# Kernel optimization log

Hardware: AMD Instinct MI355X
Metric: run time of the kernel (lower is better)

Reference implementation:

```python
import jax, jax.numpy as jnp
import numpy as np

D_IN, D_H, BATCH = 4096, 512, 8192


def _layernorm(x, g, b, eps=1e-5):
    mu = jnp.mean(x, axis=-1, keepdims=True)
    var = jnp.var(x, axis=-1, keepdims=True)
    return (x - mu) * jax.lax.rsqrt(var + eps) * g + b


def setup_inputs() -> dict:
    key = jax.random.key(0)
    ks = jax.random.split(key, 10)
    x = jax.random.normal(ks[0], (BATCH, D_IN), jnp.float32)
    h = jax.random.normal(ks[1], (BATCH, D_H), jnp.float32)
    s1 = 1.0 / np.sqrt(D_IN + D_H)
    W1 = jax.random.uniform(ks[2], (D_IN + D_H, D_H), jnp.float32, -s1, s1)
    b1 = jnp.zeros((D_H,), jnp.float32)
    ln1_g = jnp.ones((D_H,), jnp.float32)
    ln1_b = jnp.zeros((D_H,), jnp.float32)
    s2 = 1.0 / np.sqrt(D_H)
    W2 = jax.random.uniform(ks[3], (D_H, 3 * D_H), jnp.float32, -s2, s2)
    b2 = jnp.zeros((3 * D_H,), jnp.float32)
    base_tau = jnp.ones((D_H,), jnp.float32)  # time_constant_init = 1.0
    base_A = jax.random.normal(ks[4], (D_H, D_H), jnp.float32) * 0.1
    idx = jnp.arange(D_H)
    base_A = base_A.at[idx, idx].set(-0.5)
    base_B = jax.random.normal(ks[5], (D_IN, D_H), jnp.float32) * 0.1
    hn_g = jnp.ones((D_H,), jnp.float32)
    hn_b = jnp.zeros((D_H,), jnp.float32)
    return {"x": x, "h": h, "W1": W1, "b1": b1, "ln1_g": ln1_g, "ln1_b": ln1_b,
            "W2": W2, "b2": b2, "base_tau": base_tau, "base_A": base_A,
            "base_B": base_B, "hn_g": hn_g, "hn_b": hn_b}


def reference(x, h, W1, b1, ln1_g, ln1_b, W2, b2, base_tau, base_A, base_B, hn_g, hn_b):
    dt = 0.1
    # time_net hypernetwork
    xh = jnp.concatenate([x, h], axis=-1)                 # [B, D_IN+D_H]
    t = _layernorm(xh @ W1 + b1, ln1_g, ln1_b)
    t = jax.nn.gelu(t, approximate=False)
    params = t @ W2 + b2                                  # [B, 3*D_H]
    tau_s, A_s, B_s = jnp.split(params, 3, axis=-1)
    tau = base_tau * (jax.nn.sigmoid(tau_s) * 2.0)        # [B, D_H]
    A_row = 1.0 + 0.5 * jnp.tanh(A_s)                     # per-sample row scale of A
    B_col = 1.0 + 0.5 * jnp.tanh(B_s)                     # per-sample col scale of B
    # A[b] = base_A * A_row[b][:,None]; h @ A[b].T == (h @ base_A.T) * A_row[b]
    recurrent = (h @ base_A.T) * A_row                    # [B, D_H]
    # B[b] = base_B * B_col[b][None,:]; x @ B[b] == (x @ base_B) * B_col[b]
    input_term = (x @ base_B) * B_col                     # [B, D_H]
    dhdt = -h / (tau + 1e-8) + jnp.tanh(recurrent + input_term)
    new_h = _layernorm(h + dt * dhdt, hn_g, hn_b)
    return new_h
```

## Files before the change

kernel.cpp:

```cpp
#include <hip/hip_runtime.h>

#define BATCH 8192
#define DIN 4096
#define DH 512

typedef float f32x4 __attribute__((ext_vector_type(4)));
typedef float f32x2 __attribute__((ext_vector_type(2)));
typedef short s16x8 __attribute__((ext_vector_type(8)));
typedef unsigned short u16x2 __attribute__((ext_vector_type(2)));
typedef unsigned short u16x4 __attribute__((ext_vector_type(4)));
typedef unsigned short u16x8 __attribute__((ext_vector_type(8)));

static __device__ __forceinline__ unsigned short f2bf(float f) {
  unsigned int u = __float_as_uint(f);
  u += 0x7FFFu + ((u >> 16) & 1u);
  return (unsigned short)(u >> 16);
}
static __device__ __forceinline__ float bf2f(unsigned short s) {
  return __uint_as_float(((unsigned int)s) << 16);
}

typedef const __attribute__((address_space(1))) unsigned int* gas_ptr;
typedef __attribute__((address_space(3))) unsigned int* las_ptr;
static __device__ __forceinline__ void gl_lds16(const unsigned short* g, unsigned short* l) {
  __builtin_amdgcn_global_load_lds((gas_ptr)g, (las_ptr)l, 16, 0, 0);
}

static __device__ __forceinline__ void transpose_body(
    const float* __restrict__ in, int C,
    unsigned short* __restrict__ out, int ldo, int row_off,
    int bx, int by, float (*tl)[33])
{
  const int tid = threadIdx.x;
  const int tx = tid & 31, ty = tid >> 5;
  const int c0 = bx * 32, r0 = by * 32;
#pragma unroll
  for (int i = 0; i < 4; i++)
    tl[ty + 8 * i][tx] = in[(size_t)(r0 + ty + 8 * i) * C + c0 + tx];
  __syncthreads();
#pragma unroll
  for (int i = 0; i < 4; i++)
    out[(size_t)(row_off + c0 + ty + 8 * i) * ldo + r0 + tx] = f2bf(tl[tx][ty + 8 * i]);
}

__global__ __launch_bounds__(256) void prep_all_k(
    const float* __restrict__ x, unsigned short* __restrict__ xbf,
    const float* __restrict__ h, unsigned short* __restrict__ hbf,
    const float* __restrict__ base_A, unsigned short* __restrict__ Abf,
    const float* __restrict__ W1, const float* __restrict__ base_B,
    unsigned short* __restrict__ BTcat,
    const float* __restrict__ W2, unsigned short* __restrict__ W2T)
{
  __shared__ float tl[32][33];
  const int b = blockIdx.x;
  const int tid = threadIdx.x;
  const int KC = DIN + DH;
  if (b < 32768) {
    const int i = (b * 256 + tid) * 4;
    f32x4 v = *(const f32x4*)(x + i);
    u16x4 p = { f2bf(v[0]), f2bf(v[1]), f2bf(v[2]), f2bf(v[3]) };
    *(u16x4*)(xbf + i) = p;
  } else if (b < 36864) {
    const int i = ((b - 32768) * 256 + tid) * 4;
    f32x4 v = *(const f32x4*)(h + i);
    u16x4 p = { f2bf(v[0]), f2bf(v[1]), f2bf(v[2]), f2bf(v[3]) };
    *(u16x4*)(hbf + i) = p;
  } else if (b < 37120) {
    const int i = ((b - 36864) * 256 + tid) * 4;
    f32x4 v = *(const f32x4*)(base_A + i);
    u16x4 p = { f2bf(v[0]), f2bf(v[1]), f2bf(v[2]), f2bf(v[3]) };
    *(u16x4*)(Abf + i) = p;
  } else if (b < 39424) {
    const int bb = b - 37120;
    transpose_body(W1, DH, BTcat, KC, 0, bb & 15, bb >> 4, tl);
  } else if (b < 41472) {
    const int bb = b - 39424;
    transpose_body(base_B, DH, BTcat, KC, DH, bb & 15, bb >> 4, tl);
  } else if (b < 41600) {
    const int gid = (b - 41472) * 256 + tid;
    const int row = gid >> 6, c = (gid & 63) * 8;
    u16x8 z = { 0, 0, 0, 0, 0, 0, 0, 0 };
    *(u16x8*)(BTcat + (size_t)(DH + row) * KC + DIN + c) = z;
  } else {
    const int bb = b - 41600;
    transpose_body(W2, 3 * DH, W2T, DH, 0, bb % 48, bb / 48, tl);
  }
}

template<int EPI>
static __device__ __forceinline__ void gemm3_engine(
    const unsigned short* __restrict__ A0, int lda0, int K0,
    const unsigned short* __restrict__ A1, int lda1,
    const unsigned short* __restrict__ BT, int ldb,
    unsigned short* __restrict__ C0, int ldc,
    unsigned short* __restrict__ C1,
    const float* __restrict__ bias,
    const float* __restrict__ base_tau,
    int mb, int nb, int K, char* smem)
{
  unsigned short* As = (unsigned short*)smem;
  unsigned short* Bs = (unsigned short*)(smem + 16384);

  const int tid = threadIdx.x;
  const int lane = tid & 63;
  const int wid = tid >> 6;
  const int wm = (wid >> 2) * 64;
  const int wn = (wid & 3) * 64;
  const int srow = lane >> 2;
  const int scol = ((lane & 3) ^ ((lane >> 3) & 3)) * 8;
  const int fr = lane & 15;
  const int fk = ((lane >> 4) ^ ((lane >> 1) & 3)) * 8;
  const int NT = K / 32;
  const int cw = wid * 3;

  f32x4 acc[4][4];
#pragma unroll
  for (int i = 0; i < 4; i++)
#pragma unroll
    for (int j = 0; j < 4; j++)
      acc[i][j] = (f32x4){ 0.f, 0.f, 0.f, 0.f };

  auto STAGE1 = [&](int buf, int t, int j) {
    const int c = cw + j;
    const int k0 = t * 32;
    if (c < 8) {
      const bool s0 = (k0 < K0);
      const unsigned short* Ab = s0 ? A0 : A1;
      const int ld = s0 ? lda0 : lda1;
      const int ko = (s0 ? k0 : k0 - K0) + scol;
      gl_lds16(Ab + (size_t)(mb + c * 16 + srow) * ld + ko,
               As + buf * 4096 + c * 512);
    } else {
      gl_lds16(BT + (size_t)(nb + (c - 8) * 16 + srow) * ldb + k0 + scol,
               Bs + buf * 8192 + (c - 8) * 512);
    }
  };

  STAGE1(0, 0, 0); STAGE1(0, 0, 1); STAGE1(0, 0, 2);
  asm volatile("s_waitcnt vmcnt(0)" ::: "memory");
  __builtin_amdgcn_s_barrier();

  int buf = 0;
  for (int t = 0; t < NT; t++) {
    const unsigned short* ar = As + buf * 4096;
    const unsigned short* br = Bs + buf * 8192;
    s16x8 af[4], bv0, bv1, bv2, bv3;
#pragma unroll
    for (int mi = 0; mi < 4; mi++)
      af[mi] = *(const s16x8*)(ar + (wm + mi * 16 + fr) * 32 + fk);
    bv0 = *(const s16x8*)(br + (wn + 0 * 16 + fr) * 32 + fk);
    bv1 = *(const s16x8*)(br + (wn + 1 * 16 + fr) * 32 + fk);

    if (t + 1 < NT) { STAGE1(buf ^ 1, t + 1, 0); STAGE1(buf ^ 1, t + 1, 1); }

    __builtin_amdgcn_s_setprio(1);
#pragma unroll
    for (int mi = 0; mi < 4; mi++)
      acc[mi][0] = __builtin_amdgcn_mfma_f32_16x16x32_bf16(af[mi], bv0, acc[mi][0], 0, 0, 0);
#pragma unroll
    for (int mi = 0; mi < 4; mi++)
      acc[mi][1] = __builtin_amdgcn_mfma_f32_16x16x32_bf16(af[mi], bv1, acc[mi][1], 0, 0, 0);
    __builtin_amdgcn_s_setprio(0);
    __builtin_amdgcn_s_barrier();

    bv2 = *(const s16x8*)(br + (wn + 2 * 16 + fr) * 32 + fk);
    bv3 = *(const s16x8*)(br + (wn + 3 * 16 + fr) * 32 + fk);
    if (t + 1 < NT) STAGE1(buf ^ 1, t + 1, 2);

    __builtin_amdgcn_s_setprio(1);
#pragma unroll
    for (int mi = 0; mi < 4; mi++)
      acc[mi][2] = __builtin_amdgcn_mfma_f32_16x16x32_bf16(af[mi], bv2, acc[mi][2], 0, 0, 0);
#pragma unroll
    for (int mi = 0; mi < 4; mi++)
      acc[mi][3] = __builtin_amdgcn_mfma_f32_16x16x32_bf16(af[mi], bv3, acc[mi][3], 0, 0, 0);
    __builtin_amdgcn_s_setprio(0);

    asm volatile("s_waitcnt vmcnt(0) lgkmcnt(0)" ::: "memory");
    __builtin_amdgcn_sched_barrier(0);
    __builtin_amdgcn_s_barrier();
    buf ^= 1;
  }

  const int rb = (lane >> 4) * 4;
#pragma unroll
  for (int mi = 0; mi < 4; mi++) {
#pragma unroll
    for (int ni = 0; ni < 4; ni++) {
#pragma unroll
      for (int r = 0; r < 4; r++) {
        const int row = mb + wm + mi * 16 + rb + r;
        const int col = nb + wn + ni * 16 + fr;
        float v = acc[mi][ni][r];
        if (EPI == 3) {
          if (col < DH) C0[(size_t)row * DH + col] = f2bf(v + bias[col]);
          else          C1[(size_t)row * DH + (col - DH)] = f2bf(v);
        } else if (EPI == 2) {
          C0[(size_t)row * ldc + col] = f2bf(v);
        } else if (EPI == 1) {
          v += bias[col];
          if ((col >> 9) == 0) {
            const float s = 1.0f / (1.0f + expf(-v));
            v = 1.0f / (base_tau[col & (DH - 1)] * 2.0f * s + 1e-8f);
          } else {
            v = 1.0f + 0.5f * tanhf(v);
          }
          C0[(size_t)row * ldc + col] = f2bf(v);
        }
      }
    }
  }
}

template<int EPI>
static __device__ __forceinline__ void gemm2_engine(
    const unsigned short* __restrict__ A0, int lda0, int K0,
    const unsigned short* __restrict__ A1, int lda1,
    const unsigned short* __restrict__ BT, int ldb,
    unsigned short* __restrict__ C0, int ldc,
    unsigned short* __restrict__ C1,
    const float* __restrict__ bias,
    const float* __restrict__ base_tau,
    int mb, int nb, int K, char* smem)
{
  unsigned short* As = (unsigned short*)smem;
  unsigned short* Bs = (unsigned short*)(smem + 32768);
  float* red = (float*)smem;

  const int tid = threadIdx.x;
  const int lane = tid & 63;
  const int wid = tid >> 6;
  const int grp = wid >> 2;
  const int wg  = wid & 3;
  const int wm = (wg >> 1) * 64;
  const int wn = (wg & 1) * 64;
  const int srow = lane >> 2;
  const int scol = ((lane & 3) ^ ((lane >> 3) & 3)) * 8;
  const int fr = lane & 15;
  const int fk = ((lane >> 4) ^ ((lane >> 1) & 3)) * 8;
  const int NT2 = K / 64;

  f32x4 acc[4][4];
#pragma unroll
  for (int i = 0; i < 4; i++)
#pragma unroll
    for (int j = 0; j < 4; j++)
      acc[i][j] = (f32x4){ 0.f, 0.f, 0.f, 0.f };

  auto STAGE_A = [&](int buf, int per) {
    const int k0 = (2 * per + grp) * 32;
    const bool s0 = (k0 < K0);
    const unsigned short* Ab = s0 ? A0 : A1;
    const int ld = s0 ? lda0 : lda1;
    const int ko = (s0 ? k0 : k0 - K0) + scol;
    unsigned short* ab = As + (grp * 2 + buf) * 4096 + (32 * wg) * 32;
#pragma unroll
    for (int c = 0; c < 2; c++) {
      const int r = 32 * wg + c * 16 + srow;
      gl_lds16(Ab + (size_t)(mb + r) * ld + ko, ab + c * 16 * 32);
    }
  };
  auto STAGE_B = [&](int buf, int per) {
    const int k0 = (2 * per + grp) * 32;
    unsigned short* bb = Bs + (grp * 2 + buf) * 4096 + (32 * wg) * 32;
#pragma unroll
    for (int c = 0; c < 2; c++) {
      const int r = 32 * wg + c * 16 + srow;
      gl_lds16(BT + (size_t)(nb + r) * ldb + k0 + scol, bb + c * 16 * 32);
    }
  };

  STAGE_A(0, 0);
  STAGE_B(0, 0);
  asm volatile("s_waitcnt vmcnt(0)" ::: "memory");
  __builtin_amdgcn_s_barrier();

  int buf = 0;
  for (int t = 0; t < NT2; t++) {
    const unsigned short* ar = As + (grp * 2 + buf) * 4096;
    const unsigned short* br = Bs + (grp * 2 + buf) * 4096;
    s16x8 af[4], bv[4];
#pragma unroll
    for (int mi = 0; mi < 4; mi++)
      af[mi] = *(const s16x8*)(ar + (wm + mi * 16 + fr) * 32 + fk);
    bv[0] = *(const s16x8*)(br + (wn + fr) * 32 + fk);

#pragma unroll
    for (int p = 0; p < 4; p++) {
      if (p < 3)
        bv[p + 1] = *(const s16x8*)(br + (wn + (p + 1) * 16 + fr) * 32 + fk);
      if (p == 0 && t + 1 < NT2) STAGE_A(buf ^ 1, t + 1);
      if (p == 1 && t + 1 < NT2) STAGE_B(buf ^ 1, t + 1);

      __builtin_amdgcn_s_setprio(1);
#pragma unroll
      for (int mi = 0; mi < 4; mi++)
        acc[mi][p] = __builtin_amdgcn_mfma_f32_16x16x32_bf16(
            af[mi], bv[p], acc[mi][p], 0, 0, 0);
      __builtin_amdgcn_s_setprio(0);

      if (p == 3) {
        asm volatile("s_waitcnt vmcnt(0) lgkmcnt(0)" ::: "memory");
        __builtin_amdgcn_sched_barrier(0);
      }
      __builtin_amdgcn_s_barrier();
    }
    buf ^= 1;
  }

  if (grp == 1) {
#pragma unroll
    for (int mi = 0; mi < 4; mi++)
#pragma unroll
      for (int ni = 0; ni < 4; ni++)
        *(f32x4*)(red + (((wg * 4 + mi) * 4 + ni) * 64 + lane) * 4) = acc[mi][ni];
  }
  __syncthreads();
  if (grp != 0) return;

  const int rb = (lane >> 4) * 4;
#pragma unroll
  for (int mi = 0; mi < 4; mi++) {
#pragma unroll
    for (int ni = 0; ni < 4; ni++) {
      f32x4 o = *(const f32x4*)(red + (((wg * 4 + mi) * 4 + ni) * 64 + lane) * 4);
      acc[mi][ni] += o;
#pragma unroll
      for (int r = 0; r < 4; r++) {
        const int row = mb + wm + mi * 16 + rb + r;
        const int col = nb + wn + ni * 16 + fr;
        float v = acc[mi][ni][r];
        if (EPI == 2) {
          C0[(size_t)row * ldc + col] = f2bf(v);
        } else if (EPI == 1) {
          v += bias[col];
          if ((col >> 9) == 0) {
            const float s = 1.0f / (1.0f + expf(-v));
            v = 1.0f / (base_tau[col & (DH - 1)] * 2.0f * s + 1e-8f);
          } else {
            v = 1.0f + 0.5f * tanhf(v);
          }
          C0[(size_t)row * ldc + col] = f2bf(v);
        }
      }
    }
  }
}

__global__ __launch_bounds__(512) void fused_gemm_k(
    const unsigned short* __restrict__ xbf,
    const unsigned short* __restrict__ hbf,
    const unsigned short* __restrict__ BTcat,
    unsigned short* __restrict__ pre1,
    unsigned short* __restrict__ rawB,
    const float* __restrict__ b1)
{
  __shared__ __align__(16) char smem[49152];
  const int cpx = gridDim.x >> 3;
  const int virt = (blockIdx.x & 7) * cpx + (blockIdx.x >> 3);
  const int mb = (virt & 63) * 128;
  const int nb = (virt >> 6) * 256;
  gemm3_engine<3>(xbf, DIN, DIN, hbf, DH, BTcat, DIN + DH,
                  pre1, DH, rawB, b1, nullptr, mb, nb, DIN + DH, smem);
}

__global__ __launch_bounds__(512, 4) void tail_gemm_k(
    const unsigned short* __restrict__ hbf,
    const unsigned short* __restrict__ Abf,
    const unsigned short* __restrict__ tbf,
    const unsigned short* __restrict__ W2T,
    unsigned short* __restrict__ rawA,
    unsigned short* __restrict__ scales,
    const float* __restrict__ b2,
    const float* __restrict__ base_tau)
{
  __shared__ __align__(16) char smem[65536];
  const int b = blockIdx.x;
  if (b < 768) {
    const int mb = (b & 63) * 128, nb = (b >> 6) * 128;
    gemm2_engine<1>(tbf, DH, DH, nullptr, 0, W2T, DH,
                    scales, 3 * DH, nullptr, b2, base_tau, mb, nb, DH, smem);
  } else {
    const int b2i = b - 768;
    const int mb = (b2i & 63) * 128, nb = (b2i >> 6) * 128;
    gemm2_engine<2>(hbf, DH, DH, nullptr, 0, Abf, DH,
                    rawA, DH, nullptr, nullptr, nullptr, mb, nb, DH, smem);
  }
}

__device__ __forceinline__ float block_sum256(float v, float* red) {
#pragma unroll
  for (int m = 32; m >= 1; m >>= 1) v += __shfl_xor(v, m, 64);
  __syncthreads();
  if ((threadIdx.x & 63) == 0) red[threadIdx.x >> 6] = v;
  __syncthreads();
  return red[0] + red[1] + red[2] + red[3];
}

__global__ __launch_bounds__(256) void ln_gelu_k(
    const unsigned short* __restrict__ pre,
    const float* __restrict__ g, const float* __restrict__ b,
    unsigned short* __restrict__ t)
{
  __shared__ float red[4];
  const int row = blockIdx.x;
  const int c = threadIdx.x * 2;
  const size_t ro = (size_t)row * DH;
  u16x2 raw = *(const u16x2*)(pre + ro + c);
  const float v0 = bf2f(raw[0]), v1 = bf2f(raw[1]);
  const float mu = block_sum256(v0 + v1, red) * (1.0f / DH);
  const float d0 = v0 - mu, d1 = v1 - mu;
  const float var = block_sum256(d0 * d0 + d1 * d1, red) * (1.0f / DH);
  const float inv = rsqrtf(var + 1e-5f);
  const float y0 = d0 * inv * g[c] + b[c];
  const float y1 = d1 * inv * g[c + 1] + b[c + 1];
  u16x2 o = { f2bf(0.5f * y0 * (1.0f + erff(y0 * 0.70710678118f))),
              f2bf(0.5f * y1 * (1.0f + erff(y1 * 0.70710678118f))) };
  *(u16x2*)(t + ro + c) = o;
}

__global__ __launch_bounds__(256) void final_k(
    const float* __restrict__ h,
    const unsigned short* __restrict__ rawA,
    const unsigned short* __restrict__ rawB,
    const unsigned short* __restrict__ scales,
    const float* __restrict__ hn_g, const float* __restrict__ hn_b,
    float* __restrict__ out)
{
  __shared__ float red[4];
  const int row = blockIdx.x;
  const int c = threadIdx.x * 2;
  const size_t ro = (size_t)row * DH;
  f32x2 hv = *(const f32x2*)(h + ro + c);
  u16x2 ra = *(const u16x2*)(rawA + ro + c);
  u16x2 rb = *(const u16x2*)(rawB + ro + c);
  const unsigned short* sc = scales + (size_t)row * (3 * DH);
  u16x2 ti  = *(const u16x2*)(sc + c);
  u16x2 arw = *(const u16x2*)(sc + DH + c);
  u16x2 bcl = *(const u16x2*)(sc + 2 * DH + c);
  const float u0 = hv[0] + 0.1f * (-hv[0] * bf2f(ti[0])
                 + tanhf(bf2f(ra[0]) * bf2f(arw[0]) + bf2f(rb[0]) * bf2f(bcl[0])));
  const float u1 = hv[1] + 0.1f * (-hv[1] * bf2f(ti[1])
                 + tanhf(bf2f(ra[1]) * bf2f(arw[1]) + bf2f(rb[1]) * bf2f(bcl[1])));
  const float mu = block_sum256(u0 + u1, red) * (1.0f / DH);
  const float d0 = u0 - mu, d1 = u1 - mu;
  const float var = block_sum256(d0 * d0 + d1 * d1, red) * (1.0f / DH);
  const float inv = rsqrtf(var + 1e-5f);
  f32x2 o = { d0 * inv * hn_g[c] + hn_b[c],
              d1 * inv * hn_g[c + 1] + hn_b[c + 1] };
  *(f32x2*)(out + ro + c) = o;
}

extern "C" void kernel_launch(void* const* d_in, const int* in_sizes, int n_in,
                              void* d_out, int out_size, void* d_ws, size_t ws_size,
                              hipStream_t stream)
{
  const float* x        = (const float*)d_in[0];
  const float* h        = (const float*)d_in[1];
  const float* W1       = (const float*)d_in[2];
  const float* b1       = (const float*)d_in[3];
  const float* ln1_g    = (const float*)d_in[4];
  const float* ln1_b    = (const float*)d_in[5];
  const float* W2       = (const float*)d_in[6];
  const float* b2       = (const float*)d_in[7];
  const float* base_tau = (const float*)d_in[8];
  const float* base_A   = (const float*)d_in[9];
  const float* base_B   = (const float*)d_in[10];
  const float* hn_g     = (const float*)d_in[11];
  const float* hn_b     = (const float*)d_in[12];

  char* w = (char*)d_ws;
  unsigned short* xbf    = (unsigned short*)(w);
  unsigned short* hbf    = (unsigned short*)(w + 67108864);
  unsigned short* BTcat  = (unsigned short*)(w + 75497472);
  unsigned short* tbf    = (unsigned short*)(w + 75497472);
  unsigned short* W2T    = (unsigned short*)(w + 84934656);
  unsigned short* Abf    = (unsigned short*)(w + 86507520);
  unsigned short* pre1   = (unsigned short*)(w + 87031808);
  unsigned short* rawA   = (unsigned short*)(w + 87031808);
  unsigned short* rawB   = (unsigned short*)(w + 95420416);
  unsigned short* scales = (unsigned short*)(w + 103809024);

  prep_all_k<<<42368, 256, 0, stream>>>(x, xbf, h, hbf, base_A, Abf,
                                        W1, base_B, BTcat, W2, W2T);

  fused_gemm_k<<<256, 512, 0, stream>>>(xbf, hbf, BTcat, pre1, rawB, b1);
  ln_gelu_k<<<BATCH, 256, 0, stream>>>(pre1, ln1_g, ln1_b, tbf);
  tail_gemm_k<<<1024, 512, 0, stream>>>(hbf, Abf, tbf, W2T, rawA, scales, b2, base_tau);
  final_k<<<BATCH, 256, 0, stream>>>(h, rawA, rawB, scales, hn_g, hn_b, (float*)d_out);
}
```

Measured before the change: 239.3 us.

## Fuse fp32-to-bf16 conversion of x into the main GEMM with split-K warp groups

```diff
diff --git a/kernel.cpp b/kernel.cpp
--- a/kernel.cpp
+++ b/kernel.cpp
@@ -7,6 +7,7 @@
 typedef float f32x4 __attribute__((ext_vector_type(4)));
 typedef float f32x2 __attribute__((ext_vector_type(2)));
 typedef short s16x8 __attribute__((ext_vector_type(8)));
+typedef unsigned int u32x4 __attribute__((ext_vector_type(4)));
 typedef unsigned short u16x2 __attribute__((ext_vector_type(2)));
 typedef unsigned short u16x4 __attribute__((ext_vector_type(4)));
 typedef unsigned short u16x8 __attribute__((ext_vector_type(8)));
@@ -19,6 +20,11 @@
 static __device__ __forceinline__ float bf2f(unsigned short s) {
   return __uint_as_float(((unsigned int)s) << 16);
 }
+static __device__ __forceinline__ unsigned int cvtpk(float lo, float hi) {
+  unsigned int r;
+  asm("v_cvt_pk_bf16_f32 %0, %1, %2" : "=v"(r) : "v"(lo), "v"(hi));
+  return r;
+}
 
 typedef const __attribute__((address_space(1))) unsigned int* gas_ptr;
 typedef __attribute__((address_space(3))) unsigned int* las_ptr;
@@ -43,8 +49,7 @@
     out[(size_t)(row_off + c0 + ty + 8 * i) * ldo + r0 + tx] = f2bf(tl[tx][ty + 8 * i]);
 }
 
-__global__ __launch_bounds__(256) void prep_all_k(
-    const float* __restrict__ x, unsigned short* __restrict__ xbf,
+__global__ __launch_bounds__(256) void prep_small_k(
     const float* __restrict__ h, unsigned short* __restrict__ hbf,
     const float* __restrict__ base_A, unsigned short* __restrict__ Abf,
     const float* __restrict__ W1, const float* __restrict__ base_B,
@@ -55,63 +60,59 @@
   const int b = blockIdx.x;
   const int tid = threadIdx.x;
   const int KC = DIN + DH;
-  if (b < 32768) {
+  if (b < 4096) {
     const int i = (b * 256 + tid) * 4;
-    f32x4 v = *(const f32x4*)(x + i);
-    u16x4 p = { f2bf(v[0]), f2bf(v[1]), f2bf(v[2]), f2bf(v[3]) };
-    *(u16x4*)(xbf + i) = p;
-  } else if (b < 36864) {
-    const int i = ((b - 32768) * 256 + tid) * 4;
     f32x4 v = *(const f32x4*)(h + i);
     u16x4 p = { f2bf(v[0]), f2bf(v[1]), f2bf(v[2]), f2bf(v[3]) };
     *(u16x4*)(hbf + i) = p;
-  } else if (b < 37120) {
-    const int i = ((b - 36864) * 256 + tid) * 4;
+  } else if (b < 4352) {
+    const int i = ((b - 4096) * 256 + tid) * 4;
     f32x4 v = *(const f32x4*)(base_A + i);
     u16x4 p = { f2bf(v[0]), f2bf(v[1]), f2bf(v[2]), f2bf(v[3]) };
     *(u16x4*)(Abf + i) = p;
-  } else if (b < 39424) {
-    const int bb = b - 37120;
+  } else if (b < 6656) {
+    const int bb = b - 4352;
     transpose_body(W1, DH, BTcat, KC, 0, bb & 15, bb >> 4, tl);
-  } else if (b < 41472) {
-    const int bb = b - 39424;
+  } else if (b < 8704) {
+    const int bb = b - 6656;
     transpose_body(base_B, DH, BTcat, KC, DH, bb & 15, bb >> 4, tl);
-  } else if (b < 41600) {
-    const int gid = (b - 41472) * 256 + tid;
+  } else if (b < 8832) {
+    const int gid = (b - 8704) * 256 + tid;
     const int row = gid >> 6, c = (gid & 63) * 8;
     u16x8 z = { 0, 0, 0, 0, 0, 0, 0, 0 };
     *(u16x8*)(BTcat + (size_t)(DH + row) * KC + DIN + c) = z;
   } else {
-    const int bb = b - 41600;
+    const int bb = b - 8832;
     transpose_body(W2, 3 * DH, W2T, DH, 0, bb % 48, bb / 48, tl);
   }
 }
 
-template<int EPI>
-static __device__ __forceinline__ void gemm3_engine(
-    const unsigned short* __restrict__ A0, int lda0, int K0,
-    const unsigned short* __restrict__ A1, int lda1,
+static __device__ __forceinline__ void gemm2f_engine(
+    const float* __restrict__ X, int ldx, int K0,
+    const float* __restrict__ H, int ldh,
     const unsigned short* __restrict__ BT, int ldb,
-    unsigned short* __restrict__ C0, int ldc,
+    unsigned short* __restrict__ C0,
     unsigned short* __restrict__ C1,
     const float* __restrict__ bias,
-    const float* __restrict__ base_tau,
     int mb, int nb, int K, char* smem)
 {
   unsigned short* As = (unsigned short*)smem;
-  unsigned short* Bs = (unsigned short*)(smem + 16384);
+  unsigned short* Bs = (unsigned short*)(smem + 32768);
+  float* red = (float*)smem;
 
   const int tid = threadIdx.x;
   const int lane = tid & 63;
   const int wid = tid >> 6;
-  const int wm = (wid >> 2) * 64;
-  const int wn = (wid & 3) * 64;
+  const int grp = wid >> 2;
+  const int wg  = wid & 3;
+  const int wm = (wg >> 1) * 64;
+  const int wn = (wg & 1) * 64;
   const int srow = lane >> 2;
   const int scol = ((lane & 3) ^ ((lane >> 3) & 3)) * 8;
+  const int pchunk = (lane & 3) * 8;
   const int fr = lane & 15;
   const int fk = ((lane >> 4) ^ ((lane >> 1) & 3)) * 8;
-  const int NT = K / 32;
-  const int cw = wid * 3;
+  const int NT2 = K / 64;
 
   f32x4 acc[4][4];
 #pragma unroll
@@ -120,93 +121,102 @@
     for (int j = 0; j < 4; j++)
       acc[i][j] = (f32x4){ 0.f, 0.f, 0.f, 0.f };
 
-  auto STAGE1 = [&](int buf, int t, int j) {
-    const int c = cw + j;
-    const int k0 = t * 32;
-    if (c < 8) {
-      const bool s0 = (k0 < K0);
-      const unsigned short* Ab = s0 ? A0 : A1;
-      const int ld = s0 ? lda0 : lda1;
-      const int ko = (s0 ? k0 : k0 - K0) + scol;
-      gl_lds16(Ab + (size_t)(mb + c * 16 + srow) * ld + ko,
-               As + buf * 4096 + c * 512);
-    } else {
-      gl_lds16(BT + (size_t)(nb + (c - 8) * 16 + srow) * ldb + k0 + scol,
-               Bs + buf * 8192 + (c - 8) * 512);
-    }
+  f32x4 a0lo, a0hi, a1lo, a1hi;
+
+  auto ISSUE_A = [&](int per) {
+    const int k0 = (2 * per + grp) * 32;
+    const bool s0 = (k0 < K0);
+    const float* Af = s0 ? X : H;
+    const int ld = s0 ? ldx : ldh;
+    const int ko = (s0 ? k0 : k0 - K0) + scol;
+    const float* p0 = Af + (size_t)(mb + 32 * wg + srow) * ld + ko;
+    const float* p1 = Af + (size_t)(mb + 32 * wg + 16 + srow) * ld + ko;
+    a0lo = *(const f32x4*)p0;  a0hi = *(const f32x4*)(p0 + 4);
+    a1lo = *(const f32x4*)p1;  a1hi = *(const f32x4*)(p1 + 4);
   };
-
-  STAGE1(0, 0, 0); STAGE1(0, 0, 1); STAGE1(0, 0, 2);
-  asm volatile("s_waitcnt vmcnt(0)" ::: "memory");
+  auto WRITE_A = [&](int buf) {
+    unsigned short* ab = As + (grp * 2 + buf) * 4096;
+    u32x4 w0 = { cvtpk(a0lo[0], a0lo[1]), cvtpk(a0lo[2], a0lo[3]),
+                 cvtpk(a0hi[0], a0hi[1]), cvtpk(a0hi[2], a0hi[3]) };
+    u32x4 w1 = { cvtpk(a1lo[0], a1lo[1]), cvtpk(a1lo[2], a1lo[3]),
+                 cvtpk(a1hi[0], a1hi[1]), cvtpk(a1hi[2], a1hi[3]) };
+    *(u32x4*)(ab + (32 * wg + srow) * 32 + pchunk) = w0;
+    *(u32x4*)(ab + (32 * wg + 16 + srow) * 32 + pchunk) = w1;
+  };
+  auto STAGE_B = [&](int buf, int per) {
+    const int k0 = (2 * per + grp) * 32;
+    unsigned short* bb = Bs + (grp * 2 + buf) * 4096 + (32 * wg) * 32;
+#pragma unroll
+    for (int c = 0; c < 2; c++) {
+      const int r = 32 * wg + c * 16 + srow;
+      gl_lds16(BT + (size_t)(nb + r) * ldb + k0 + scol, bb + c * 16 * 32);
+    }
+  };
+
+  ISSUE_A(0);
+  STAGE_B(0, 0);
+  WRITE_A(0);
+  asm volatile("s_waitcnt vmcnt(0) lgkmcnt(0)" ::: "memory");
   __builtin_amdgcn_s_barrier();
 
   int buf = 0;
-  for (int t = 0; t < NT; t++) {
-    const unsigned short* ar = As + buf * 4096;
-    const unsigned short* br = Bs + buf * 8192;
-    s16x8 af[4], bv0, bv1, bv2, bv3;
+  for (int t = 0; t < NT2; t++) {
+    const unsigned short* ar = As + (grp * 2 + buf) * 4096;
+    const unsigned short* br = Bs + (grp * 2 + buf) * 4096;
+    s16x8 af[4], bv[4];
 #pragma unroll
     for (int mi = 0; mi < 4; mi++)
       af[mi] = *(const s16x8*)(ar + (wm + mi * 16 + fr) * 32 + fk);
-    bv0 = *(const s16x8*)(br + (wn + 0 * 16 + fr) * 32 + fk);
-    bv1 = *(const s16x8*)(br + (wn + 1 * 16 + fr) * 32 + fk);
-
-    if (t + 1 < NT) { STAGE1(buf ^ 1, t + 1, 0); STAGE1(buf ^ 1, t + 1, 1); }
-
-    __builtin_amdgcn_s_setprio(1);
+    bv[0] = *(const s16x8*)(br + (wn + fr) * 32 + fk);
+
+#pragma unroll
+    for (int p = 0; p < 4; p++) {
+      if (p < 3)
+        bv[p + 1] = *(const s16x8*)(br + (wn + (p + 1) * 16 + fr) * 32 + fk);
+      if (p == 0 && t + 1 < NT2) ISSUE_A(t + 1);
+      if (p == 1 && t + 1 < NT2) STAGE_B(buf ^ 1, t + 1);
+      if (p == 3 && t + 1 < NT2) WRITE_A(buf ^ 1);
+
+      __builtin_amdgcn_s_setprio(1);
+#pragma unroll
+      for (int mi = 0; mi < 4; mi++)
+        acc[mi][p] = __builtin_amdgcn_mfma_f32_16x16x32_bf16(
+            af[mi], bv[p], acc[mi][p], 0, 0, 0);
+      __builtin_amdgcn_s_setprio(0);
+
+      if (p == 3) {
+        asm volatile("s_waitcnt vmcnt(0) lgkmcnt(0)" ::: "memory");
+        __builtin_amdgcn_sched_barrier(0);
+      }
+      __builtin_amdgcn_s_barrier();
+    }
+    buf ^= 1;
+  }
+
+  if (grp == 1) {
 #pragma unroll
     for (int mi = 0; mi < 4; mi++)
-      acc[mi][0] = __builtin_amdgcn_mfma_f32_16x16x32_bf16(af[mi], bv0, acc[mi][0], 0, 0, 0);
-#pragma unroll
-    for (int mi = 0; mi < 4; mi++)
-      acc[mi][1] = __builtin_amdgcn_mfma_f32_16x16x32_bf16(af[mi], bv1, acc[mi][1], 0, 0, 0);
-    __builtin_amdgcn_s_setprio(0);
-    __builtin_amdgcn_s_barrier();
-
-    bv2 = *(const s16x8*)(br + (wn + 2 * 16 + fr) * 32 + fk);
-    bv3 = *(const s16x8*)(br + (wn + 3 * 16 + fr) * 32 + fk);
-    if (t + 1 < NT) STAGE1(buf ^ 1, t + 1, 2);
-
-    __builtin_amdgcn_s_setprio(1);
-#pragma unroll
-    for (int mi = 0; mi < 4; mi++)
-      acc[mi][2] = __builtin_amdgcn_mfma_f32_16x16x32_bf16(af[mi], bv2, acc[mi][2], 0, 0, 0);
-#pragma unroll
-    for (int mi = 0; mi < 4; mi++)
-      acc[mi][3] = __builtin_amdgcn_mfma_f32_16x16x32_bf16(af[mi], bv3, acc[mi][3], 0, 0, 0);
-    __builtin_amdgcn_s_setprio(0);
-
-    asm volatile("s_waitcnt vmcnt(0) lgkmcnt(0)" ::: "memory");
-    __builtin_amdgcn_sched_barrier(0);
-    __builtin_amdgcn_s_barrier();
-    buf ^= 1;
-  }
+#pragma unroll
+      for (int ni = 0; ni < 4; ni++)
+        *(f32x4*)(red + (((wg * 4 + mi) * 4 + ni) * 64 + lane) * 4) = acc[mi][ni];
+  }
+  __syncthreads();
+  if (grp != 0) return;
 
   const int rb = (lane >> 4) * 4;
 #pragma unroll
   for (int mi = 0; mi < 4; mi++) {
 #pragma unroll
     for (int ni = 0; ni < 4; ni++) {
+      f32x4 o = *(const f32x4*)(red + (((wg * 4 + mi) * 4 + ni) * 64 + lane) * 4);
+      acc[mi][ni] += o;
 #pragma unroll
       for (int r = 0; r < 4; r++) {
         const int row = mb + wm + mi * 16 + rb + r;
         const int col = nb + wn + ni * 16 + fr;
         float v = acc[mi][ni][r];
-        if (EPI == 3) {
-          if (col < DH) C0[(size_t)row * DH + col] = f2bf(v + bias[col]);
-          else          C1[(size_t)row * DH + (col - DH)] = f2bf(v);
-        } else if (EPI == 2) {
-          C0[(size_t)row * ldc + col] = f2bf(v);
-        } else if (EPI == 1) {
-          v += bias[col];
-          if ((col >> 9) == 0) {
-            const float s = 1.0f / (1.0f + expf(-v));
-            v = 1.0f / (base_tau[col & (DH - 1)] * 2.0f * s + 1e-8f);
-          } else {
-            v = 1.0f + 0.5f * tanhf(v);
-          }
-          C0[(size_t)row * ldc + col] = f2bf(v);
-        }
+        if (col < DH) C0[(size_t)row * DH + col] = f2bf(v + bias[col]);
+        else          C1[(size_t)row * DH + (col - DH)] = f2bf(v);
       }
     }
   }
@@ -347,21 +357,21 @@
   }
 }
 
-__global__ __launch_bounds__(512) void fused_gemm_k(
-    const unsigned short* __restrict__ xbf,
-    const unsigned short* __restrict__ hbf,
+__global__ __launch_bounds__(512, 4) void fused_gemm_k(
+    const float* __restrict__ x,
+    const float* __restrict__ h,
     const unsigned short* __restrict__ BTcat,
     unsigned short* __restrict__ pre1,
     unsigned short* __restrict__ rawB,
     const float* __restrict__ b1)
 {
-  __shared__ __align__(16) char smem[49152];
+  __shared__ __align__(16) char smem[65536];
   const int cpx = gridDim.x >> 3;
   const int virt = (blockIdx.x & 7) * cpx + (blockIdx.x >> 3);
   const int mb = (virt & 63) * 128;
-  const int nb = (virt >> 6) * 256;
-  gemm3_engine<3>(xbf, DIN, DIN, hbf, DH, BTcat, DIN + DH,
-                  pre1, DH, rawB, b1, nullptr, mb, nb, DIN + DH, smem);
+  const int nb = (virt >> 6) * 128;
+  gemm2f_engine(x, DIN, DIN, h, DH, BTcat, DIN + DH,
+                pre1, rawB, b1, mb, nb, DIN + DH, smem);
 }
 
 __global__ __launch_bounds__(512, 4) void tail_gemm_k(
@@ -470,7 +480,6 @@
   const float* hn_b     = (const float*)d_in[12];
 
   char* w = (char*)d_ws;
-  unsigned short* xbf    = (unsigned short*)(w);
   unsigned short* hbf    = (unsigned short*)(w + 67108864);
   unsigned short* BTcat  = (unsigned short*)(w + 75497472);
   unsigned short* tbf    = (unsigned short*)(w + 75497472);
@@ -481,10 +490,10 @@
   unsigned short* rawB   = (unsigned short*)(w + 95420416);
   unsigned short* scales = (unsigned short*)(w + 103809024);
 
-  prep_all_k<<<42368, 256, 0, stream>>>(x, xbf, h, hbf, base_A, Abf,
-                                        W1, base_B, BTcat, W2, W2T);
-
-  fused_gemm_k<<<256, 512, 0, stream>>>(xbf, hbf, BTcat, pre1, rawB, b1);
+  prep_small_k<<<9600, 256, 0, stream>>>(h, hbf, base_A, Abf,
+                                         W1, base_B, BTcat, W2, W2T);
+
+  fused_gemm_k<<<512, 512, 0, stream>>>(x, h, BTcat, pre1, rawB, b1);
   ln_gelu_k<<<BATCH, 256, 0, stream>>>(pre1, ln1_g, ln1_b, tbf);
   tail_gemm_k<<<1024, 512, 0, stream>>>(hbf, Abf, tbf, W2T, rawA, scales, b2, base_tau);
   final_k<<<BATCH, 256, 0, stream>>>(h, rawA, rawB, scales, hn_g, hn_b, (float*)d_out);
```

After: 291.2 us. 1.22x slower.
